# Kernel optimization log

Measured on AMD Instinct MI355X. Metric: run time of the kernel, lower is better.

Reference implementation:

```python
import jax, jax.numpy as jnp
import numpy as np

B, S, H, I, E, K = 4, 1024, 1024, 2048, 8, 2  # batch, seq, hidden, intermediate, experts, top-k


def setup_inputs() -> dict:
    key = jax.random.key(0)
    ks = jax.random.split(key, 9)
    sd = 0.02
    return {
        "x": jax.random.normal(ks[0], (B, S, H), jnp.float32),
        "gate_w": jax.random.normal(ks[1], (E, H), jnp.float32) * (H ** -0.5),
        "expert_bias": jnp.zeros((E,), jnp.float32),  # e_expert_biases (aux-free LB)
        "Wg": jax.random.normal(ks[2], (E, H, I), jnp.float32) * sd,
        "Wu": jax.random.normal(ks[3], (E, H, I), jnp.float32) * sd,
        "Wd": jax.random.normal(ks[4], (E, I, H), jnp.float32) * sd,
        "Sg": jax.random.normal(ks[5], (H, I), jnp.float32) * sd,
        "Su": jax.random.normal(ks[6], (H, I), jnp.float32) * sd,
        "Sd": jax.random.normal(ks[7], (I, H), jnp.float32) * sd,
    }


def _swiglu(x, wg, wu, wd):
    # down( silu(gate(x)) * up(x) )
    return (jax.nn.silu(x @ wg) * (x @ wu)) @ wd


def reference(x, gate_w, expert_bias, Wg, Wu, Wd, Sg, Su, Sd):
    b, s, h = x.shape
    shared = _swiglu(x, Sg, Su, Sd)  # single shared expert, applied to all tokens

    xf = x.reshape(b * s, h)                      # [T,H]
    scores = xf @ gate_w.T                        # [T,E]
    _, idx = jax.lax.top_k(scores + expert_bias, K)   # selection uses biased scores
    rp, _ = jax.lax.top_k(scores, K)              # weights use raw top-k scores (as in source)
    w = jax.nn.sigmoid(rp)
    w = w / jnp.sum(w, axis=-1, keepdims=True)    # [T,K]

    # per-expert combine weight: cw[t,e] = sum_j w[t,j] * 1[idx[t,j]==e]
    cw = jnp.sum(jax.nn.one_hot(idx, E, dtype=x.dtype) * w[..., None], axis=1)  # [T,E]

    out = jnp.zeros_like(xf)
    for e in range(E):  # fixed small loop over experts (dense equivalent of grouped dispatch)
        out = out + cw[:, e:e + 1] * _swiglu(xf, Wg[e], Wu[e], Wd[e])
    out = out.reshape(b, s, h) + shared

    # maximal violation (detached routing statistic)
    freq = jnp.zeros((E,), x.dtype).at[idx.reshape(-1)].add(1.0) / idx.size
    viol = (freq.max() - freq.mean()) / freq.mean()
    return out, viol
```

## Files before the change

kernel.cpp:

```cpp
#include <hip/hip_runtime.h>
#include <hip/hip_bf16.h>

#define T_TOK 4096
#define HD 1024
#define ID 2048
#define NE 8

typedef __attribute__((ext_vector_type(8))) __bf16 bf16x8;
typedef __attribute__((ext_vector_type(4))) float f32x4;
typedef __attribute__((ext_vector_type(4))) unsigned int u32x4;
typedef __attribute__((ext_vector_type(2))) unsigned int u32x2;

#define AS1 __attribute__((address_space(1)))
#define AS3 __attribute__((address_space(3)))

#define WAITV(N) asm volatile("s_waitcnt vmcnt(" #N ")" ::: "memory")
#define BAR()    asm volatile("s_barrier" ::: "memory")
#define LGKM0()  { asm volatile("s_waitcnt lgkmcnt(0)" ::: "memory"); __builtin_amdgcn_sched_barrier(0); }

__device__ __forceinline__ unsigned short f2bf(float f) {
  __hip_bfloat16 h = __float2bfloat16(f);
  return __builtin_bit_cast(unsigned short, h);
}
__device__ __forceinline__ unsigned int pk2(float lo, float hi) {
  return (unsigned int)f2bf(lo) | ((unsigned int)f2bf(hi) << 16);
}
__device__ __forceinline__ float bflo(unsigned int u) { return __builtin_bit_cast(float, u << 16); }
__device__ __forceinline__ float bfhi(unsigned int u) { return __builtin_bit_cast(float, u & 0xffff0000u); }
__device__ __forceinline__ void gl16(const void* g, void* l) {
  __builtin_amdgcn_global_load_lds((const AS1 unsigned int*)g, (AS3 unsigned int*)l, 16, 0, 0);
}

__global__ void k_zero(int* cnt) { if (threadIdx.x < 32) cnt[threadIdx.x] = 0; }

__device__ __forceinline__ void route_block(int rbid, const float* __restrict__ x,
    const float* __restrict__ gw, const float* __restrict__ bias,
    int* __restrict__ cnt, int* __restrict__ tokens, float* __restrict__ wts,
    int* __restrict__ slotrec, unsigned short* __restrict__ xb, unsigned short* __restrict__ tl)
{
  int* lcnt  = (int*)tl;
  int* gbase = lcnt + 8;
  int* pe    = gbase + 8;
  int* pr    = pe + 32;
  int* pt    = pr + 32;
  float* pw  = (float*)(pt + 32);
  const int tid = threadIdx.x, lane = tid & 63, wv = tid >> 6;
  if (tid < 8) lcnt[tid] = 0;
  __syncthreads();
  #pragma unroll
  for (int i = 0; i < 4; ++i) {
    const int t = rbid * 16 + wv * 4 + i;
    const float* xr = x + (size_t)t * HD + lane * 16;
    f32x4 xv[4];
    #pragma unroll
    for (int j = 0; j < 4; ++j) xv[j] = *(const f32x4*)(xr + j * 4);
    {
      u32x4 p0 = { pk2(xv[0][0],xv[0][1]), pk2(xv[0][2],xv[0][3]), pk2(xv[1][0],xv[1][1]), pk2(xv[1][2],xv[1][3]) };
      u32x4 p1 = { pk2(xv[2][0],xv[2][1]), pk2(xv[2][2],xv[2][3]), pk2(xv[3][0],xv[3][1]), pk2(xv[3][2],xv[3][3]) };
      unsigned short* xd = xb + (size_t)t * HD + lane * 16;
      *(u32x4*)xd = p0;
      *(u32x4*)(xd + 8) = p1;
    }
    float sc[NE];
    #pragma unroll
    for (int e = 0; e < NE; ++e) {
      const float* gr = gw + e * HD + lane * 16;
      float a = 0.f;
      #pragma unroll
      for (int j = 0; j < 4; ++j) {
        f32x4 gv = *(const f32x4*)(gr + j * 4);
        a += xv[j][0]*gv[0] + xv[j][1]*gv[1] + xv[j][2]*gv[2] + xv[j][3]*gv[3];
      }
      #pragma unroll
      for (int off = 32; off > 0; off >>= 1) a += __shfl_xor(a, off);
      sc[e] = a;
    }
    int i1 = 0; float b1 = sc[0] + bias[0];
    #pragma unroll
    for (int e = 1; e < NE; ++e) { float be = sc[e] + bias[e]; if (be > b1) { b1 = be; i1 = e; } }
    int i2 = -1; float b2 = -3e38f;
    #pragma unroll
    for (int e = 0; e < NE; ++e) { if (e == i1) continue; float be = sc[e] + bias[e]; if (be > b2) { b2 = be; i2 = e; } }
    int a1 = 0; float r1 = sc[0];
    #pragma unroll
    for (int e = 1; e < NE; ++e) if (sc[e] > r1) { r1 = sc[e]; a1 = e; }
    float r2 = -3e38f;
    #pragma unroll
    for (int e = 0; e < NE; ++e) if (e != a1 && sc[e] > r2) r2 = sc[e];
    float w1 = 1.f / (1.f + __expf(-r1));
    float w2 = 1.f / (1.f + __expf(-r2));
    float s = w1 + w2; w1 /= s; w2 /= s;
    if (lane == 0) {
      int pk = wv * 8 + i * 2;
      int q1 = atomicAdd(&lcnt[i1], 1);
      pe[pk] = i1; pr[pk] = q1; pt[pk] = t; pw[pk] = w1;
      int q2 = atomicAdd(&lcnt[i2], 1);
      pe[pk+1] = i2; pr[pk+1] = q2; pt[pk+1] = t; pw[pk+1] = w2;
    }
  }
  __syncthreads();
  if (tid < 8) gbase[tid] = atomicAdd(&cnt[tid], lcnt[tid]);
  __syncthreads();
  if (tid < 32) {
    int e = pe[tid], p = gbase[e] + pr[tid];
    tokens[e * T_TOK + p] = pt[tid];
    wts[e * T_TOK + p] = pw[tid];
    slotrec[pt[tid] * 2 + (tid & 1)] = (e << 16) | p;
  }
}

__global__ void k_fin(const int* __restrict__ cnt, int* __restrict__ base, float* __restrict__ out)
{
  if (threadIdx.x == 0) {
    int b = 0, mx = 0;
    #pragma unroll
    for (int e = 0; e < NE; ++e) { base[e] = b; b += cnt[e]; if (cnt[e] > mx) mx = cnt[e]; }
    base[NE] = b;
    out[(size_t)T_TOK * HD] = (float)mx * (1.f / 1024.f) - 1.f;
  }
}

__device__ __forceinline__ void tcvt_tile(const float* __restrict__ src, unsigned short* __restrict__ dst,
                                          int K, int N, int mode, int k0, int n0, unsigned short* tl)
{
  const int t = threadIdx.x;
  const int nc = (t & 15) * 4;
  #pragma unroll
  for (int it = 0; it < 4; ++it) {
    int kr = (t >> 4) + it * 16;
    f32x4 v = *(const f32x4*)&src[(size_t)(k0 + kr) * N + n0 + nc];
    #pragma unroll
    for (int j = 0; j < 4; ++j) {
      int n = nc + j;
      int g = (n ^ (n >> 2)) & 7;
      tl[n * 64 + (((kr >> 3) ^ g) * 8) + (kr & 7)] = f2bf(v[j]);
    }
  }
  __syncthreads();
  #pragma unroll
  for (int it = 0; it < 2; ++it) {
    int idx = t + it * 256;
    int n = idx >> 3, kc8 = idx & 7;
    int g = (n ^ (n >> 2)) & 7;
    u32x4 v = *(const u32x4*)&tl[n * 64 + ((kc8 ^ g) * 8)];
    int nn = n0 + n;
    int vrow = (mode == 0) ? nn : (((nn >> 5) << 6) + (nn & 31) + ((mode == 2) ? 32 : 0));
    *(u32x4*)&dst[(size_t)vrow * K + k0 + kc8 * 8] = v;
  }
}

__global__ __launch_bounds__(256) void k_conv(const float* __restrict__ x,
    const float* __restrict__ gw, const float* __restrict__ bias,
    const float* __restrict__ Wg, const float* __restrict__ Wu,
    const float* __restrict__ Sg, const float* __restrict__ Su,
    const float* __restrict__ Wd, const float* __restrict__ Sd,
    unsigned short* __restrict__ xb, unsigned short* __restrict__ Wgu, unsigned short* __restrict__ Sgu,
    unsigned short* __restrict__ WdT, unsigned short* __restrict__ SdT,
    int* __restrict__ cnt, int* __restrict__ tokens, float* __restrict__ wts, int* __restrict__ slotrec)
{
  __shared__ __attribute__((aligned(16))) unsigned short tl[64 * 64];
  int bid = blockIdx.x;
  if (bid < 9216) {
    int z = bid >> 9, rem = bid & 511;
    int bx = rem & 31, by = rem >> 5;
    const float* src; unsigned short* dst; int mode;
    if (z < 8)        { src = Wg + (size_t)z * HD * ID;       dst = Wgu + (size_t)z * 4096 * 1024; mode = 1; }
    else if (z < 16)  { src = Wu + (size_t)(z - 8) * HD * ID; dst = Wgu + (size_t)(z - 8) * 4096 * 1024; mode = 2; }
    else if (z == 16) { src = Sg; dst = Sgu; mode = 1; }
    else              { src = Su; dst = Sgu; mode = 2; }
    tcvt_tile(src, dst, HD, ID, mode, by * 64, bx * 64, tl);
    return;
  }
  bid -= 9216;
  if (bid < 4608) {
    int z = bid >> 9, rem = bid & 511;
    int bx = rem & 15, by = rem >> 4;
    const float* src = (z < 8) ? Wd + (size_t)z * ID * HD : Sd;
    unsigned short* dst = (z < 8) ? WdT + (size_t)z * ID * HD : SdT;
    tcvt_tile(src, dst, ID, HD, 0, by * 64, bx * 64, tl);
    return;
  }
  bid -= 4608;
  route_block(bid, x, gw, bias, cnt, tokens, wts, slotrec, xb, tl);
}

__device__ __forceinline__ int chunked_vid(int bid, int total) {
  int xcd = bid & 7, idx = bid >> 3;
  int q = total >> 3, r = total & 7;
  int cap = (xcd < r) ? q + 1 : q;
  if (idx >= cap) return -1;
  int base = (xcd < r) ? xcd * (q + 1) : r * (q + 1) + (xcd - r) * q;
  return base + idx;
}

__global__ __launch_bounds__(512, 2) void k_mlp1(
    const unsigned short* __restrict__ xb,
    const unsigned short* __restrict__ Wgu, const unsigned short* __restrict__ Sgu,
    const int* __restrict__ cnt, const int* __restrict__ base, const int* __restrict__ tokens,
    unsigned short* __restrict__ act)
{
  __shared__ __attribute__((aligned(16))) unsigned short Abuf[2][16384];
  __shared__ __attribute__((aligned(16))) unsigned short Bbuf[2][16384];

  int total = 0;
  #pragma unroll
  for (int ee = 0; ee < 9; ++ee) {
    int c = (ee == 8) ? T_TOK : cnt[ee];
    total += ((c + 255) >> 8) * 16;
  }
  const int vid = chunked_vid(blockIdx.x, total);
  if (vid < 0) return;
  int e = -1, loc = vid, amv = 1;
  #pragma unroll
  for (int ee = 0; ee < 9; ++ee) {
    int c = (ee == 8) ? T_TOK : cnt[ee];
    int a = (c + 255) >> 8;
    int sz = a * 16;
    if (e < 0) { if (loc < sz) { e = ee; amv = a; } else loc -= sz; }
  }
  int nx = 0; while (loc >= amv) { loc -= amv; ++nx; }
  const int my = loc;

  const int cntE = (e == NE) ? T_TOK : cnt[e];
  const int m0 = my * 256;
  const int n0 = nx * 256;
  const unsigned short* Bsrc = (e == NE) ? Sgu : Wgu + (size_t)e * 4096 * 1024;
  const int rowbase = (e == NE) ? 2 * T_TOK : base[e];
  const int tid = threadIdx.x, lane = tid & 63, w = tid >> 6;
  const int srow = tid >> 3;
  const int kgf = (tid & 7) ^ (srow & 7);

  const unsigned short* asrc[4]; const unsigned short* bsrc[4];
  #pragma unroll
  for (int u = 0; u < 4; ++u) {
    int r = u * 64 + srow;
    int rl = min(m0 + r, cntE - 1);
    int tok = (e == NE) ? rl : tokens[e * T_TOK + rl];
    asrc[u] = xb + (size_t)tok * HD + kgf * 8;
    bsrc[u] = Bsrc + (size_t)(n0 + r) * HD + kgf * 8;
  }

  f32x4 acc[8][4];
  const f32x4 z4 = {0.f, 0.f, 0.f, 0.f};
  #pragma unroll
  for (int i = 0; i < 8; ++i)
    #pragma unroll
    for (int j = 0; j < 4; ++j) acc[i][j] = z4;

  const int lr = lane & 15, lg = lane >> 4;
  const int wm = (w >> 2) * 128;
  const int wn4 = (w & 3) * 64;
  const int ck0 = (lg ^ (lr & 7)) * 16;
  const int arow0 = (wm + lr) * 128;
  const int brow0 = (wn4 + lr) * 128;

  bf16x8 af[4][2], bf[2][2][2];

  #define SA1(t_, h_, s_) { \
    gl16(asrc[(h_)*2+0] + (t_)*64, &Abuf[s_][(h_)*8192 + 0    + w*512]); \
    gl16(asrc[(h_)*2+1] + (t_)*64, &Abuf[s_][(h_)*8192 + 4096 + w*512]); }
  #define SB1(t_, h_, s_) { \
    gl16(bsrc[(h_)*2+0] + (t_)*64, &Bbuf[s_][(h_)*8192 + 0    + w*512]); \
    gl16(bsrc[(h_)*2+1] + (t_)*64, &Bbuf[s_][(h_)*8192 + 4096 + w*512]); }
  #define LDA1(s_, mh_) { _Pragma("unroll") for (int am_ = 0; am_ < 4; ++am_) { \
    af[am_][0] = *(const bf16x8*)((const char*)&Abuf[s_][0] + arow0 + (mh_)*8192 + am_*2048 + ck0); \
    af[am_][1] = *(const bf16x8*)((const char*)&Abuf[s_][0] + arow0 + (mh_)*8192 + am_*2048 + (ck0^64)); } }
  #define LDB1(s_, nh_) { _Pragma("unroll") for (int bn_ = 0; bn_ < 2; ++bn_) { \
    bf[nh_][bn_][0] = *(const bf16x8*)((const char*)&Bbuf[s_][0] + brow0 + (nh_)*4096 + bn_*2048 + ck0); \
    bf[nh_][bn_][1] = *(const bf16x8*)((const char*)&Bbuf[s_][0] + brow0 + (nh_)*4096 + bn_*2048 + (ck0^64)); } }
  #define MM1(mh_, nh_) { __builtin_amdgcn_s_setprio(1); \
    _Pragma("unroll") for (int bn_ = 0; bn_ < 2; ++bn_) \
      _Pragma("unroll") for (int am_ = 0; am_ < 4; ++am_) { \
        acc[(mh_)*4+am_][(nh_)*2+bn_] = __builtin_amdgcn_mfma_f32_16x16x32_bf16(af[am_][0], bf[nh_][bn_][0], acc[(mh_)*4+am_][(nh_)*2+bn_], 0,0,0); \
        acc[(mh_)*4+am_][(nh_)*2+bn_] = __builtin_amdgcn_mfma_f32_16x16x32_bf16(af[am_][1], bf[nh_][bn_][1], acc[(mh_)*4+am_][(nh_)*2+bn_], 0,0,0); } \
    __builtin_amdgcn_s_setprio(0); }

  const int NT1 = 16;
  SA1(0, 0, 0); SA1(0, 1, 0); SB1(0, 0, 0); SB1(0, 1, 0);
  SB1(1, 0, 1); SB1(1, 1, 1);
  WAITV(4);
  BAR();

  #define TILE1(t_, s_, o_) { \
    LDA1(s_, 0); LDB1(s_, 0); LDB1(s_, 1); \
    if ((t_)+1 < NT1) { SA1((t_)+1, 0, o_); SA1((t_)+1, 1, o_); } \
    BAR(); LGKM0(); MM1(0, 0); MM1(0, 1); BAR(); \
    LDA1(s_, 1); \
    if ((t_)+2 < NT1) { SB1((t_)+2, 0, s_); SB1((t_)+2, 1, s_); } \
    BAR(); LGKM0(); MM1(1, 1); MM1(1, 0); \
    if ((t_)+2 < NT1) { WAITV(4); } else { WAITV(0); } \
    BAR(); }

  for (int t = 0; t < NT1; t += 2) {
    TILE1(t, 0, 1);
    TILE1(t + 1, 1, 0);
  }
  #undef TILE1

  const int colbase = ((n0 + wn4) >> 1);
  #pragma unroll
  for (int mf = 0; mf < 8; ++mf) {
    const int rloc = wm + (mf >> 2) * 64 + (mf & 3) * 16 + lg * 4;
    #pragma unroll
    for (int p = 0; p < 2; ++p) {
      f32x4 gv = acc[mf][p], uv = acc[mf][p + 2];
      int col = colbase + p * 16 + lr;
      #pragma unroll
      for (int q = 0; q < 4; ++q) {
        int r = rloc + q;
        if (m0 + r < cntE) {
          float g_ = gv[q], u_ = uv[q];
          act[(size_t)(rowbase + m0 + r) * ID + col] = f2bf((g_ / (1.f + __expf(-g_))) * u_);
        }
      }
    }
  }
}

__global__ __launch_bounds__(512, 2) void k_mlp2(
    const unsigned short* __restrict__ act,
    const unsigned short* __restrict__ WdT, const unsigned short* __restrict__ SdT,
    const int* __restrict__ cnt, const int* __restrict__ base,
    unsigned short* __restrict__ dn0, unsigned short* __restrict__ dn1)
{
  __shared__ __attribute__((aligned(16))) unsigned short Abuf[2][16384];
  __shared__ __attribute__((aligned(16))) unsigned short Bbuf[2][16384];

  int total = 0;
  #pragma unroll
  for (int ee = 0; ee < 9; ++ee) {
    int c = (ee == 8) ? T_TOK : cnt[ee];
    total += ((c + 255) >> 8) * 8;
  }
  const int vid = chunked_vid(blockIdx.x, total);
  if (vid < 0) return;
  int e = -1, loc = vid, amv = 1;
  #pragma unroll
  for (int ee = 0; ee < 9; ++ee) {
    int c = (ee == 8) ? T_TOK : cnt[ee];
    int a = (c + 255) >> 8;
    int sz = a * 8;
    if (e < 0) { if (loc < sz) { e = ee; amv = a; } else loc -= sz; }
  }
  int nxkh = 0; while (loc >= amv) { loc -= amv; ++nxkh; }
  const int my = loc;
  const int nx = nxkh >> 1, kh = nxkh & 1;

  const int cntE = (e == NE) ? T_TOK : cnt[e];
  const int m0 = my * 256;
  const int n0 = nx * 256;
  const unsigned short* Bsrc = (e == NE) ? SdT : WdT + (size_t)e * ID * HD;
  const int rowbase = (e == NE) ? 2 * T_TOK : base[e];
  const int koff = kh * 1024;
  const int tid = threadIdx.x, lane = tid & 63, w = tid >> 6;
  const int srow = tid >> 3;
  const int kgf = (tid & 7) ^ (srow & 7);

  const unsigned short* asrc[4]; const unsigned short* bsrc[4];
  #pragma unroll
  for (int u = 0; u < 4; ++u) {
    int r = u * 64 + srow;
    int rl = rowbase + min(m0 + r, cntE - 1);
    asrc[u] = act + (size_t)rl * ID + koff + kgf * 8;
    bsrc[u] = Bsrc + (size_t)(n0 + r) * ID + koff + kgf * 8;
  }

  f32x4 acc[8][4];
  const f32x4 z4 = {0.f, 0.f, 0.f, 0.f};
  #pragma unroll
  for (int i = 0; i < 8; ++i)
    #pragma unroll
    for (int j = 0; j < 4; ++j) acc[i][j] = z4;

  const int lr = lane & 15, lg = lane >> 4;
  const int wm = (w >> 2) * 128;
  const int wn4 = (w & 3) * 64;
  const int ck0 = (lg ^ (lr & 7)) * 16;
  const int arow0 = (wm + lr) * 128;
  const int brow0 = (wn4 + lr) * 128;

  bf16x8 af[4][2], bf[2][2][2];

  #define SA2(t_, h_, s_) { \
    gl16(asrc[(h_)*2+0] + (t_)*64, &Abuf[s_][(h_)*8192 + 0    + w*512]); \
    gl16(asrc[(h_)*2+1] + (t_)*64, &Abuf[s_][(h_)*8192 + 4096 + w*512]); }
  #define SB2(t_, h_, s_) { \
    gl16(bsrc[(h_)*2+0] + (t_)*64, &Bbuf[s_][(h_)*8192 + 0    + w*512]); \
    gl16(bsrc[(h_)*2+1] + (t_)*64, &Bbuf[s_][(h_)*8192 + 4096 + w*512]); }
  #define LDA2(s_, mh_) { _Pragma("unroll") for (int am_ = 0; am_ < 4; ++am_) { \
    af[am_][0] = *(const bf16x8*)((const char*)&Abuf[s_][0] + arow0 + (mh_)*8192 + am_*2048 + ck0); \
    af[am_][1] = *(const bf16x8*)((const char*)&Abuf[s_][0] + arow0 + (mh_)*8192 + am_*2048 + (ck0^64)); } }
  #define LDB2(s_, nh_) { _Pragma("unroll") for (int bn_ = 0; bn_ < 2; ++bn_) { \
    bf[nh_][bn_][0] = *(const bf16x8*)((const char*)&Bbuf[s_][0] + brow0 + (nh_)*4096 + bn_*2048 + ck0); \
    bf[nh_][bn_][1] = *(const bf16x8*)((const char*)&Bbuf[s_][0] + brow0 + (nh_)*4096 + bn_*2048 + (ck0^64)); } }
  #define MM2(mh_, nh_) { __builtin_amdgcn_s_setprio(1); \
    _Pragma("unroll") for (int bn_ = 0; bn_ < 2; ++bn_) \
      _Pragma("unroll") for (int am_ = 0; am_ < 4; ++am_) { \
        acc[(mh_)*4+am_][(nh_)*2+bn_] = __builtin_amdgcn_mfma_f32_16x16x32_bf16(af[am_][0], bf[nh_][bn_][0], acc[(mh_)*4+am_][(nh_)*2+bn_], 0,0,0); \
        acc[(mh_)*4+am_][(nh_)*2+bn_] = __builtin_amdgcn_mfma_f32_16x16x32_bf16(af[am_][1], bf[nh_][bn_][1], acc[(mh_)*4+am_][(nh_)*2+bn_], 0,0,0); } \
    __builtin_amdgcn_s_setprio(0); }

  const int NT2 = 16;
  SA2(0, 0, 0); SA2(0, 1, 0); SB2(0, 0, 0); SB2(0, 1, 0);
  SB2(1, 0, 1); SB2(1, 1, 1);
  WAITV(4);
  BAR();

  #define TILE2(t_, s_, o_) { \
    LDA2(s_, 0); LDB2(s_, 0); LDB2(s_, 1); \
    if ((t_)+1 < NT2) { SA2((t_)+1, 0, o_); SA2((t_)+1, 1, o_); } \
    BAR(); LGKM0(); MM2(0, 0); MM2(0, 1); BAR(); \
    LDA2(s_, 1); \
    if ((t_)+2 < NT2) { SB2((t_)+2, 0, s_); SB2((t_)+2, 1, s_); } \
    BAR(); LGKM0(); MM2(1, 1); MM2(1, 0); \
    if ((t_)+2 < NT2) { WAITV(4); } else { WAITV(0); } \
    BAR(); }

  for (int t = 0; t < NT2; t += 2) {
    TILE2(t, 0, 1);
    TILE2(t + 1, 1, 0);
  }
  #undef TILE2
  #undef SA2
  #undef SB2
  #undef LDA2
  #undef LDB2
  #undef MM2
  #undef SA1
  #undef SB1
  #undef LDA1
  #undef LDB1
  #undef MM1

  unsigned short* dnp = kh ? dn1 : dn0;
  #pragma unroll
  for (int mf = 0; mf < 8; ++mf) {
    const int rloc = wm + (mf >> 2) * 64 + (mf & 3) * 16 + lg * 4;
    #pragma unroll
    for (int nf = 0; nf < 4; ++nf) {
      f32x4 av = acc[mf][nf];
      int col = n0 + wn4 + nf * 16 + lr;
      #pragma unroll
      for (int q = 0; q < 4; ++q) {
        int r = rloc + q;
        if (m0 + r < cntE)
          dnp[(size_t)(rowbase + m0 + r) * HD + col] = f2bf(av[q]);
      }
    }
  }
}

__global__ __launch_bounds__(256) void k_comb(const unsigned short* __restrict__ dn0,
    const unsigned short* __restrict__ dn1,
    const int* __restrict__ base, const int* __restrict__ slotrec,
    const float* __restrict__ wts, float* __restrict__ out)
{
  const int t = blockIdx.x;
  const int c = threadIdx.x * 4;
  int r0 = slotrec[t * 2], r1 = slotrec[t * 2 + 1];
  int e0 = r0 >> 16, p0 = r0 & 0xffff;
  int e1 = r1 >> 16, p1 = r1 & 0xffff;
  size_t s0 = (size_t)(base[e0] + p0) * HD + c;
  size_t s1 = (size_t)(base[e1] + p1) * HD + c;
  size_t sh = (size_t)(2 * T_TOK + t) * HD + c;
  float w0 = wts[e0 * T_TOK + p0], w1 = wts[e1 * T_TOK + p1];
  u32x2 vs0 = *(const u32x2*)&dn0[sh], vs1 = *(const u32x2*)&dn1[sh];
  u32x2 va0 = *(const u32x2*)&dn0[s0], va1 = *(const u32x2*)&dn1[s0];
  u32x2 vb0 = *(const u32x2*)&dn0[s1], vb1 = *(const u32x2*)&dn1[s1];
  f32x4 o;
  o[0] = (bflo(vs0[0]) + bflo(vs1[0])) + w0 * (bflo(va0[0]) + bflo(va1[0])) + w1 * (bflo(vb0[0]) + bflo(vb1[0]));
  o[1] = (bfhi(vs0[0]) + bfhi(vs1[0])) + w0 * (bfhi(va0[0]) + bfhi(va1[0])) + w1 * (bfhi(vb0[0]) + bfhi(vb1[0]));
  o[2] = (bflo(vs0[1]) + bflo(vs1[1])) + w0 * (bflo(va0[1]) + bflo(va1[1])) + w1 * (bflo(vb0[1]) + bflo(vb1[1]));
  o[3] = (bfhi(vs0[1]) + bfhi(vs1[1])) + w0 * (bfhi(va0[1]) + bfhi(va1[1])) + w1 * (bfhi(vb0[1]) + bfhi(vb1[1]));
  *(f32x4*)&out[(size_t)t * HD + c] = o;
}

extern "C" void kernel_launch(void* const* d_in, const int* in_sizes, int n_in,
                              void* d_out, int out_size, void* d_ws, size_t ws_size,
                              hipStream_t stream)
{
  const float* x    = (const float*)d_in[0];
  const float* gw   = (const float*)d_in[1];
  const float* bias = (const float*)d_in[2];
  const float* Wg   = (const float*)d_in[3];
  const float* Wu   = (const float*)d_in[4];
  const float* Wd   = (const float*)d_in[5];
  const float* Sg   = (const float*)d_in[6];
  const float* Su   = (const float*)d_in[7];
  const float* Sd   = (const float*)d_in[8];
  float* out = (float*)d_out;
  char* ws = (char*)d_ws;

  int*   cnt     = (int*)ws;
  int*   base    = cnt + 16;
  int*   tokens  = (int*)(ws + 512);
  float* wts     = (float*)(ws + 512 + (NE * T_TOK * 4));
  int*   slotrec = (int*)(ws + 512 + 2 * (NE * T_TOK * 4));

  const size_t MB = (size_t)1 << 20;
  unsigned short* xbf = (unsigned short*)(ws + 1 * MB);
  unsigned short* WdT = (unsigned short*)(ws + 9 * MB);
  unsigned short* SdT = (unsigned short*)(ws + 41 * MB);
  unsigned short* Wgu = (unsigned short*)(ws + 45 * MB);
  unsigned short* Sgu = (unsigned short*)(ws + 109 * MB);
  unsigned short* actb = (unsigned short*)(ws + 117 * MB);
  unsigned short* dn0 = (unsigned short*)(ws + 45 * MB);
  unsigned short* dn1 = (unsigned short*)(ws + 69 * MB);

  k_zero<<<dim3(1), dim3(64), 0, stream>>>(cnt);
  k_conv<<<dim3(9216 + 4608 + 256), dim3(256), 0, stream>>>(
      x, gw, bias, Wg, Wu, Sg, Su, Wd, Sd,
      xbf, Wgu, Sgu, WdT, SdT, cnt, tokens, wts, slotrec);
  k_fin<<<dim3(1), dim3(64), 0, stream>>>(cnt, base, out);
  k_mlp1<<<dim3(2304), dim3(512), 0, stream>>>(xbf, Wgu, Sgu, cnt, base, tokens, actb);
  k_mlp2<<<dim3(1152), dim3(512), 0, stream>>>(actb, WdT, SdT, cnt, base, dn0, dn1);
  k_comb<<<dim3(T_TOK), dim3(256), 0, stream>>>(dn0, dn1, base, slotrec, wts, out);
}
```

Before: 289.2 us.

## Move down-projection weight conversion into the first MLP kernel's tail blocks

The fp32-to-bf16 transpose conversion of Wd and Sd moves out of the preprocessing kernel and into extra blocks appended to the gate/up GEMM launch, using a 512-thread tile converter. The aim is to overlap that bandwidth-bound conversion with the tail of the compute-bound GEMM and shorten the conversion kernel. The trade-off is that the conversion blocks take 64KB-LDS GEMM slots and may delay GEMM blocks or contend for memory bandwidth.

Measured after the change: 281.6 us. 1.03x faster.

```diff
diff --git a/kernel.cpp b/kernel.cpp
--- a/kernel.cpp
+++ b/kernel.cpp
@@ -149,13 +149,36 @@
   }
 }
 
+__device__ __forceinline__ void tcvt_tile512(const float* __restrict__ src, unsigned short* __restrict__ dst,
+                                             int K, int N, int k0, int n0, unsigned short* tl)
+{
+  const int t = threadIdx.x;
+  const int nc = (t & 15) * 4;
+  #pragma unroll
+  for (int it = 0; it < 2; ++it) {
+    int kr = (t >> 4) + it * 32;
+    f32x4 v = *(const f32x4*)&src[(size_t)(k0 + kr) * N + n0 + nc];
+    #pragma unroll
+    for (int j = 0; j < 4; ++j) {
+      int n = nc + j;
+      int g = (n ^ (n >> 2)) & 7;
+      tl[n * 64 + (((kr >> 3) ^ g) * 8) + (kr & 7)] = f2bf(v[j]);
+    }
+  }
+  __syncthreads();
+  {
+    int n = t >> 3, kc8 = t & 7;
+    int g = (n ^ (n >> 2)) & 7;
+    u32x4 v = *(const u32x4*)&tl[n * 64 + ((kc8 ^ g) * 8)];
+    *(u32x4*)&dst[(size_t)(n0 + n) * K + k0 + kc8 * 8] = v;
+  }
+}
+
 __global__ __launch_bounds__(256) void k_conv(const float* __restrict__ x,
     const float* __restrict__ gw, const float* __restrict__ bias,
     const float* __restrict__ Wg, const float* __restrict__ Wu,
     const float* __restrict__ Sg, const float* __restrict__ Su,
-    const float* __restrict__ Wd, const float* __restrict__ Sd,
     unsigned short* __restrict__ xb, unsigned short* __restrict__ Wgu, unsigned short* __restrict__ Sgu,
-    unsigned short* __restrict__ WdT, unsigned short* __restrict__ SdT,
     int* __restrict__ cnt, int* __restrict__ tokens, float* __restrict__ wts, int* __restrict__ slotrec)
 {
   __shared__ __attribute__((aligned(16))) unsigned short tl[64 * 64];
@@ -172,15 +195,6 @@
     return;
   }
   bid -= 9216;
-  if (bid < 4608) {
-    int z = bid >> 9, rem = bid & 511;
-    int bx = rem & 15, by = rem >> 4;
-    const float* src = (z < 8) ? Wd + (size_t)z * ID * HD : Sd;
-    unsigned short* dst = (z < 8) ? WdT + (size_t)z * ID * HD : SdT;
-    tcvt_tile(src, dst, ID, HD, 0, by * 64, bx * 64, tl);
-    return;
-  }
-  bid -= 4608;
   route_block(bid, x, gw, bias, cnt, tokens, wts, slotrec, xb, tl);
 }
 
@@ -196,11 +210,23 @@
 __global__ __launch_bounds__(512, 2) void k_mlp1(
     const unsigned short* __restrict__ xb,
     const unsigned short* __restrict__ Wgu, const unsigned short* __restrict__ Sgu,
+    const float* __restrict__ Wd, const float* __restrict__ Sd,
+    unsigned short* __restrict__ WdT, unsigned short* __restrict__ SdT,
     const int* __restrict__ cnt, const int* __restrict__ base, const int* __restrict__ tokens,
     unsigned short* __restrict__ act)
 {
   __shared__ __attribute__((aligned(16))) unsigned short Abuf[2][16384];
   __shared__ __attribute__((aligned(16))) unsigned short Bbuf[2][16384];
+
+  if (blockIdx.x >= 2304) {
+    int bid = blockIdx.x - 2304;
+    int z = bid >> 9, rem = bid & 511;
+    int bx = rem & 15, by = rem >> 4;
+    const float* src = (z < 8) ? Wd + (size_t)z * ID * HD : Sd;
+    unsigned short* dst = (z < 8) ? WdT + (size_t)z * ID * HD : SdT;
+    tcvt_tile512(src, dst, ID, HD, by * 64, bx * 64, &Abuf[0][0]);
+    return;
+  }
 
   int total = 0;
   #pragma unroll
@@ -508,11 +534,11 @@
   unsigned short* dn1 = (unsigned short*)(ws + 69 * MB);
 
   k_zero<<<dim3(1), dim3(64), 0, stream>>>(cnt);
-  k_conv<<<dim3(9216 + 4608 + 256), dim3(256), 0, stream>>>(
-      x, gw, bias, Wg, Wu, Sg, Su, Wd, Sd,
-      xbf, Wgu, Sgu, WdT, SdT, cnt, tokens, wts, slotrec);
+  k_conv<<<dim3(9216 + 256), dim3(256), 0, stream>>>(
+      x, gw, bias, Wg, Wu, Sg, Su,
+      xbf, Wgu, Sgu, cnt, tokens, wts, slotrec);
   k_fin<<<dim3(1), dim3(64), 0, stream>>>(cnt, base, out);
-  k_mlp1<<<dim3(2304), dim3(512), 0, stream>>>(xbf, Wgu, Sgu, cnt, base, tokens, actb);
+  k_mlp1<<<dim3(2304 + 4608), dim3(512), 0, stream>>>(xbf, Wgu, Sgu, Wd, Sd, WdT, SdT, cnt, base, tokens, actb);
   k_mlp2<<<dim3(1152), dim3(512), 0, stream>>>(actb, WdT, SdT, cnt, base, dn0, dn1);
   k_comb<<<dim3(T_TOK), dim3(256), 0, stream>>>(dn0, dn1, base, slotrec, wts, out);
 }
```
